# Optimization experiments

Hardware: AMD Instinct MI355X
Metric: run time of the kernel (lower is better)

## Reference

```python
import jax, jax.numpy as jnp
import numpy as np

B, D_MODEL, N, H = 4, 256, 2048, 4
HEAD_DIM = D_MODEL // H  # 64


def _rotate_half(x):
    # x: [..., d] with d even; pairs (x1, x2) -> (-x2, x1)
    x = x.reshape(x.shape[:-1] + (x.shape[-1] // 2, 2))
    x1, x2 = x[..., 0], x[..., 1]
    return jnp.stack((-x2, x1), axis=-1).reshape(x.shape[:-2] + (-1,))


def _apply_rope(freqs, t):
    # freqs: [2, n, d] (cos, sin); t: [b, h, n, d]
    return t * freqs[0] + _rotate_half(t) * freqs[1]


def setup_inputs() -> dict:
    key = jax.random.key(0)
    ks = jax.random.split(key, 12)
    s = 0.02
    inp = {
        "query": jax.random.normal(ks[0], (B, D_MODEL, N), jnp.float32),
        "key": jax.random.normal(ks[1], (B, D_MODEL, N), jnp.float32),
        "value": jax.random.normal(ks[2], (B, D_MODEL, N), jnp.float32),
        "encoding": jax.random.normal(ks[3], (2, N, HEAD_DIM), jnp.float32),
        "Wq": jax.random.normal(ks[4], (D_MODEL, D_MODEL), jnp.float32) * s,
        "bq": jnp.zeros((D_MODEL,), jnp.float32),
        "Wk": jax.random.normal(ks[5], (D_MODEL, D_MODEL), jnp.float32) * s,
        "bk": jnp.zeros((D_MODEL,), jnp.float32),
        "Wv": jax.random.normal(ks[6], (D_MODEL, D_MODEL), jnp.float32) * s,
        "bv": jnp.zeros((D_MODEL,), jnp.float32),
        "Wm": jax.random.normal(ks[7], (D_MODEL, D_MODEL), jnp.float32) * s,
        "bm": jnp.zeros((D_MODEL,), jnp.float32),
    }
    return inp


def _proj(W, b, x):
    # 1x1 Conv1d == channel matmul: x [b, c_in, n] -> [b, c_out, n]
    return jnp.einsum('oi,bin->bon', W, x) + b[None, :, None]


def reference(query, key, value, encoding, Wq, bq, Wk, bk, Wv, bv, Wm, bm):
    b = query.shape[0]
    # project and split channels into (head_dim, heads): [b, d, h, n]
    q = _proj(Wq, bq, query).reshape(b, HEAD_DIM, H, -1)
    k = _proj(Wk, bk, key).reshape(b, HEAD_DIM, H, -1)
    v = _proj(Wv, bv, value).reshape(b, HEAD_DIM, H, -1)
    # RoPE on [b, h, n, d] layout
    q = jnp.transpose(_apply_rope(encoding, jnp.transpose(q, (0, 2, 3, 1))), (0, 3, 1, 2))
    k = jnp.transpose(_apply_rope(encoding, jnp.transpose(k, (0, 2, 3, 1))), (0, 3, 1, 2))
    # attention: scores [b, h, n, m]
    scores = jnp.einsum('bdhn,bdhm->bhnm', q, k) / jnp.sqrt(jnp.float32(HEAD_DIM))
    prob = jax.nn.softmax(scores, axis=-1)
    x = jnp.einsum('bhnm,bdhm->bdhn', prob, v)
    x = x.reshape(b, HEAD_DIM * H, -1)
    return _proj(Wm, bm, x)
```

## Files before the change

kernel.cpp:

```cpp
#include <hip/hip_runtime.h>
#include <stdint.h>

#define NSEQ 2048

typedef __attribute__((ext_vector_type(4))) float f32x4;
typedef __attribute__((ext_vector_type(8))) short s16x8;
typedef _Float16 f16x8 __attribute__((ext_vector_type(8)));

#define OFF_XT  0u
#define OFF_PO  0u
#define OFF_M   16777216u
#define OFF_L   17301504u
#define OFF_QR  17825792u
#define OFF_KR  22020096u
#define OFF_VT  26214400u

__device__ __forceinline__ short f2h(float f) {
  _Float16 h = (_Float16)f;
  return __builtin_bit_cast(short, h);
}
__device__ __forceinline__ float h2f(short s) {
  return (float)__builtin_bit_cast(_Float16, s);
}
__device__ __forceinline__ int swz128(int row, int slot) {
  return row * 128 + ((slot ^ (row & 7)) << 4);
}
#define MFMA(a, b, c) __builtin_amdgcn_mfma_f32_16x16x32_f16(a, b, c, 0, 0, 0)

__global__ __launch_bounds__(256) void k_trans(const float* __restrict__ q,
    const float* __restrict__ k, const float* __restrict__ v, char* __restrict__ ws) {
  int tensor = blockIdx.z >> 2, b = blockIdx.z & 3;
  const float* src = tensor == 0 ? q : (tensor == 1 ? k : v);
  short* dst = (short*)(ws + OFF_XT) + (tensor * 4 + b) * 524288;
  int n0 = blockIdx.x * 64, i0 = blockIdx.y * 64;
  __shared__ float tile[64][65];
  int t = threadIdx.x;
  int nl = t & 63, ib = (t >> 6) * 16;
#pragma unroll
  for (int r = 0; r < 16; ++r)
    tile[ib + r][nl] = src[(b * 256 + i0 + ib + r) * 2048 + n0 + nl];
  __syncthreads();
  int nr = t >> 2, ic = (t & 3) * 16;
  short tmp[16];
#pragma unroll
  for (int j = 0; j < 16; ++j) tmp[j] = f2h(tile[ic + j][nr]);
  short* dp = &dst[(n0 + nr) * 256 + i0 + ic];
  *(s16x8*)dp = *(const s16x8*)&tmp[0];
  *(s16x8*)(dp + 8) = *(const s16x8*)&tmp[8];
}

__global__ __launch_bounds__(256) void k_proj(const float* __restrict__ Wq,
    const float* __restrict__ Wk, const float* __restrict__ Wv,
    const float* __restrict__ enc, const float* __restrict__ bq,
    const float* __restrict__ bk, const float* __restrict__ bv, char* __restrict__ ws) {
  int proj = blockIdx.z >> 2, b = blockIdx.z & 3;
  const float* W = proj == 0 ? Wq : (proj == 1 ? Wk : Wv);
  const short* X = (const short*)(ws + OFF_XT) + (proj * 4 + b) * 524288;
  int o0 = blockIdx.y * 64, n0 = blockIdx.x * 64;
  __shared__ short As[64 * 64], Bs[64 * 64];
  int t = threadIdx.x, lane = t & 63, g = lane >> 4, c = lane & 15, wave = t >> 6;
  int wr = wave >> 1, wc = wave & 1;
  int row = t >> 2, seg = t & 3;
  f32x4 acc[2][2] = {};
  for (int kk = 0; kk < 4; ++kk) {
    __syncthreads();
    int koff = kk * 64;
    const float* wsrc = &W[(o0 + row) * 256 + koff + seg * 16];
    short ha[16];
#pragma unroll
    for (int q4 = 0; q4 < 4; ++q4) {
      f32x4 wv4 = *(const f32x4*)(wsrc + q4 * 4);
#pragma unroll
      for (int j = 0; j < 4; ++j) ha[q4 * 4 + j] = f2h(wv4[j]);
    }
    *(s16x8*)((char*)As + swz128(row, seg * 2))     = *(const s16x8*)&ha[0];
    *(s16x8*)((char*)As + swz128(row, seg * 2 + 1)) = *(const s16x8*)&ha[8];
    const short* xsrc = &X[(n0 + row) * 256 + koff];
    *(s16x8*)((char*)Bs + swz128(row, seg))     = *(const s16x8*)(xsrc + seg * 8);
    *(s16x8*)((char*)Bs + swz128(row, 4 + seg)) = *(const s16x8*)(xsrc + 32 + seg * 8);
    __syncthreads();
#pragma unroll
    for (int ks = 0; ks < 2; ++ks) {
      f16x8 af[2], bfr[2];
#pragma unroll
      for (int f = 0; f < 2; ++f) {
        af[f]  = *(const f16x8*)((char*)As + swz128(wr * 32 + f * 16 + c, ks * 4 + g));
        bfr[f] = *(const f16x8*)((char*)Bs + swz128(wc * 32 + f * 16 + c, ks * 4 + g));
      }
#pragma unroll
      for (int i = 0; i < 2; ++i)
#pragma unroll
        for (int j = 0; j < 2; ++j)
          acc[i][j] = MFMA(af[i], bfr[j], acc[i][j]);
    }
  }
  const float* bias = proj == 0 ? bq : (proj == 1 ? bk : bv);
  if (proj < 2) {
    short* dst0 = (short*)(ws + (proj == 0 ? OFF_QR : OFF_KR));
    float scale = proj == 0 ? 0.18033688f : 1.0f;
    float sgn = (g & 1) ? 1.0f : -1.0f;
#pragma unroll
    for (int i = 0; i < 2; ++i) {
      int ob = o0 + wr * 32 + i * 16 + g * 4;
      int d = ob >> 2;
#pragma unroll
      for (int j = 0; j < 2; ++j) {
        int n = n0 + wc * 32 + j * 16 + c;
        float cv = enc[n * 64 + d], sv = enc[131072 + n * 64 + d];
#pragma unroll
        for (int r = 0; r < 4; ++r) {
          float val = acc[i][j][r] + bias[ob + r];
          float par = __shfl_xor(val, 16, 64);
          float res = (val * cv + sgn * par * sv) * scale;
          dst0[((b * 4 + r) * 2048 + n) * 64 + d] = f2h(res);
        }
      }
    }
  } else {
    short* dst = (short*)(ws + OFF_VT);
#pragma unroll
    for (int i = 0; i < 2; ++i) {
      int ob = o0 + wr * 32 + i * 16 + g * 4;
      int d = ob >> 2;
#pragma unroll
      for (int j = 0; j < 2; ++j) {
        int n = n0 + wc * 32 + j * 16 + c;
#pragma unroll
        for (int r = 0; r < 4; ++r) {
          float val = acc[i][j][r] + bias[ob + r];
          dst[((b * 4 + r) * 64 + d) * 2048 + n] = f2h(val);
        }
      }
    }
  }
}

__global__ __launch_bounds__(256, 4) void k_attn(char* __restrict__ ws) {
  int bh = blockIdx.y, ms = blockIdx.z;
  int t = threadIdx.x, wave = t >> 6, lane = t & 63, g = lane >> 4, c = lane & 15;
  int nw = blockIdx.x * 64 + wave * 16;
  const short* Q = (const short*)(ws + OFF_QR) + bh * 131072;
  const short* K = (const short*)(ws + OFF_KR) + bh * 131072;
  const short* V = (const short*)(ws + OFF_VT) + bh * 131072;
  __shared__ short Ks[64 * 64], Vs[64 * 64], Ps[4][16 * 64];
  char* Pb = (char*)Ps[wave];
  f16x8 qf0 = *(const f16x8*)&Q[(nw + c) * 64 + g * 8];
  f16x8 qf1 = *(const f16x8*)&Q[(nw + c) * 64 + 32 + g * 8];
  f32x4 po[4] = {};
  float mrun = -1e30f, lrun = 0.f;
  int sr = t >> 3, sl = t & 7;
  const int mb = ms * 512;
  int bsrc = g * 16 + g * 4;

  s16x8 RA[4], RB[4];
  auto LD = [&](int m0, s16x8* R) {
    R[0] = *(const s16x8*)&K[(m0 + sr) * 64 + sl * 8];
    R[1] = *(const s16x8*)&K[(m0 + sr + 32) * 64 + sl * 8];
    R[2] = *(const s16x8*)&V[sr * 2048 + m0 + sl * 8];
    R[3] = *(const s16x8*)&V[(sr + 32) * 2048 + m0 + sl * 8];
  };
  auto ST = [&](const s16x8* R) {
    *(s16x8*)((char*)Ks + swz128(sr, sl))      = R[0];
    *(s16x8*)((char*)Ks + swz128(sr + 32, sl)) = R[1];
    *(s16x8*)((char*)Vs + swz128(sr, sl))      = R[2];
    *(s16x8*)((char*)Vs + swz128(sr + 32, sl)) = R[3];
  };
  auto COMPUTE = [&]() {
    f32x4 s[4] = {};
    __builtin_amdgcn_s_setprio(1);
#pragma unroll
    for (int fj = 0; fj < 4; ++fj) {
      f16x8 k0 = *(const f16x8*)((char*)Ks + swz128(fj * 16 + c, g));
      f16x8 k1 = *(const f16x8*)((char*)Ks + swz128(fj * 16 + c, 4 + g));
      s[fj] = MFMA(k0, qf0, s[fj]);
      s[fj] = MFMA(k1, qf1, s[fj]);
    }
    __builtin_amdgcn_s_setprio(0);
    float t0 = fmaxf(fmaxf(s[0][0], s[0][1]), fmaxf(s[0][2], s[0][3]));
    float t1 = fmaxf(fmaxf(s[1][0], s[1][1]), fmaxf(s[1][2], s[1][3]));
    float t2 = fmaxf(fmaxf(s[2][0], s[2][1]), fmaxf(s[2][2], s[2][3]));
    float t3 = fmaxf(fmaxf(s[3][0], s[3][1]), fmaxf(s[3][2], s[3][3]));
    float rmax = fmaxf(fmaxf(t0, t1), fmaxf(t2, t3));
    rmax = fmaxf(rmax, __shfl_xor(rmax, 16, 64));
    rmax = fmaxf(rmax, __shfl_xor(rmax, 32, 64));
    if (__any(rmax > mrun + 11.5f)) {
      float nm = fmaxf(mrun, rmax);
      float corr = exp2f(mrun - nm);
      mrun = nm;
      lrun *= corr;
#pragma unroll
      for (int r = 0; r < 4; ++r) {
        float corr_r = __shfl(corr, bsrc + r, 64);
#pragma unroll
        for (int fd = 0; fd < 4; ++fd) po[fd][r] *= corr_r;
      }
    }
    float p[4][4], rs = 0.f;
#pragma unroll
    for (int fj = 0; fj < 4; ++fj) {
      f32x4 pv;
#pragma unroll
      for (int r = 0; r < 4; ++r) {
        pv[r] = exp2f(s[fj][r] - mrun);
        p[fj][r] = pv[r];
      }
      rs += (pv[0] + pv[1]) + (pv[2] + pv[3]);
    }
    rs += __shfl_xor(rs, 16, 64);
    rs += __shfl_xor(rs, 32, 64);
    lrun += rs;
#pragma unroll
    for (int fj = 0; fj < 4; ++fj)
#pragma unroll
      for (int r = 0; r < 4; ++r) {
        int mm = fj * 16 + g * 4 + r;
        *(short*)(Pb + swz128(c, mm >> 3) + (mm & 7) * 2) = f2h(p[fj][r]);
      }
    asm volatile("s_waitcnt lgkmcnt(0)" ::: "memory");
    __builtin_amdgcn_sched_barrier(0);
    f16x8 pa0 = *(const f16x8*)(Pb + swz128(c, g));
    f16x8 pa1 = *(const f16x8*)(Pb + swz128(c, 4 + g));
    __builtin_amdgcn_s_setprio(1);
#pragma unroll
    for (int fd = 0; fd < 4; ++fd) {
      int dd = fd * 16 + c;
      f16x8 vb0 = *(const f16x8*)((char*)Vs + swz128(dd, g));
      f16x8 vb1 = *(const f16x8*)((char*)Vs + swz128(dd, 4 + g));
      po[fd] = MFMA(pa0, vb0, po[fd]);
      po[fd] = MFMA(pa1, vb1, po[fd]);
    }
    __builtin_amdgcn_s_setprio(0);
  };

  LD(mb, RA);
  for (int tt = 0; tt < 8; tt += 2) {
    __syncthreads();
    ST(RA);
    LD(mb + (tt + 1) * 64, RB);
    __syncthreads();
    COMPUTE();
    __syncthreads();
    ST(RB);
    if (tt + 2 < 8) LD(mb + (tt + 2) * 64, RA);
    __syncthreads();
    COMPUTE();
  }

  short* PO = (short*)(ws + OFF_PO);
  float* Mm = (float*)(ws + OFF_M);
  float* Ll = (float*)(ws + OFF_L);
  int base = (ms * 16 + bh) * 2048;
  float li[4];
#pragma unroll
  for (int r = 0; r < 4; ++r) li[r] = 1.0f / __shfl(lrun, bsrc + r, 64);
#pragma unroll
  for (int fd = 0; fd < 4; ++fd) {
    int d = fd * 16 + c;
#pragma unroll
    for (int r = 0; r < 4; ++r) {
      int n = nw + g * 4 + r;
      PO[(base + n) * 64 + d] = f2h(po[fd][r] * li[r]);
    }
  }
  if (g == 0) {
    Mm[base + nw + c] = mrun;
    Ll[base + nw + c] = lrun;
  }
}

__global__ __launch_bounds__(256) void k_final(const float* __restrict__ Wm,
    const float* __restrict__ bm, float* __restrict__ out, char* __restrict__ ws) {
  int b = blockIdx.z;
  int o0 = blockIdx.y * 64, n0 = blockIdx.x * 64;
  const short* PO = (const short*)(ws + OFF_PO);
  const float* Mm = (const float*)(ws + OFF_M);
  const float* Ll = (const float*)(ws + OFF_L);
  __shared__ short As[64 * 64], Bs[64 * 64];
  int t = threadIdx.x, lane = t & 63, g = lane >> 4, c = lane & 15, wave = t >> 6;
  int wr = wave >> 1, wc = wave & 1;
  int row = t >> 2, seg = t & 3;
  f32x4 acc[2][2] = {};
  for (int kk = 0; kk < 4; ++kk) {
    __syncthreads();
    short ha[16];
#pragma unroll
    for (int j = 0; j < 16; ++j)
      ha[j] = f2h(Wm[(o0 + row) * 256 + (seg * 16 + j) * 4 + kk]);
    *(s16x8*)((char*)As + swz128(row, seg * 2))     = *(const s16x8*)&ha[0];
    *(s16x8*)((char*)As + swz128(row, seg * 2 + 1)) = *(const s16x8*)&ha[8];
    int bh = b * 4 + kk;
    int nr = n0 + row;
    float m0 = Mm[(0 * 16 + bh) * 2048 + nr], l0 = Ll[(0 * 16 + bh) * 2048 + nr];
    float m1 = Mm[(1 * 16 + bh) * 2048 + nr], l1 = Ll[(1 * 16 + bh) * 2048 + nr];
    float m2 = Mm[(2 * 16 + bh) * 2048 + nr], l2 = Ll[(2 * 16 + bh) * 2048 + nr];
    float m3 = Mm[(3 * 16 + bh) * 2048 + nr], l3 = Ll[(3 * 16 + bh) * 2048 + nr];
    float M = fmaxf(fmaxf(m0, m1), fmaxf(m2, m3));
    float w0 = l0 * exp2f(m0 - M), w1 = l1 * exp2f(m1 - M);
    float w2 = l2 * exp2f(m2 - M), w3 = l3 * exp2f(m3 - M);
    float inv = 1.f / (w0 + w1 + w2 + w3);
    w0 *= inv; w1 *= inv; w2 *= inv; w3 *= inv;
    float cb[16];
    {
      const short* p0 = &PO[((0 * 16 + bh) * 2048 + nr) * 64 + seg * 16];
      const short* p1 = &PO[((1 * 16 + bh) * 2048 + nr) * 64 + seg * 16];
      const short* p2 = &PO[((2 * 16 + bh) * 2048 + nr) * 64 + seg * 16];
      const short* p3 = &PO[((3 * 16 + bh) * 2048 + nr) * 64 + seg * 16];
      s16x8 a0 = *(const s16x8*)p0, a1 = *(const s16x8*)(p0 + 8);
      s16x8 b0 = *(const s16x8*)p1, b1 = *(const s16x8*)(p1 + 8);
      s16x8 c0 = *(const s16x8*)p2, c1 = *(const s16x8*)(p2 + 8);
      s16x8 d0 = *(const s16x8*)p3, d1 = *(const s16x8*)(p3 + 8);
#pragma unroll
      for (int j = 0; j < 8; ++j) {
        cb[j]     = w0 * h2f(a0[j]) + w1 * h2f(b0[j]) + w2 * h2f(c0[j]) + w3 * h2f(d0[j]);
        cb[j + 8] = w0 * h2f(a1[j]) + w1 * h2f(b1[j]) + w2 * h2f(c1[j]) + w3 * h2f(d1[j]);
      }
    }
    short hb[16];
#pragma unroll
    for (int j = 0; j < 16; ++j) hb[j] = f2h(cb[j]);
    *(s16x8*)((char*)Bs + swz128(row, seg * 2))     = *(const s16x8*)&hb[0];
    *(s16x8*)((char*)Bs + swz128(row, seg * 2 + 1)) = *(const s16x8*)&hb[8];
    __syncthreads();
#pragma unroll
    for (int ks = 0; ks < 2; ++ks) {
      f16x8 af[2], bfr[2];
#pragma unroll
      for (int f = 0; f < 2; ++f) {
        af[f]  = *(const f16x8*)((char*)As + swz128(wr * 32 + f * 16 + c, ks * 4 + g));
        bfr[f] = *(const f16x8*)((char*)Bs + swz128(wc * 32 + f * 16 + c, ks * 4 + g));
      }
#pragma unroll
      for (int i = 0; i < 2; ++i)
#pragma unroll
        for (int j = 0; j < 2; ++j)
          acc[i][j] = MFMA(af[i], bfr[j], acc[i][j]);
    }
  }
#pragma unroll
  for (int i = 0; i < 2; ++i) {
    int ob = o0 + wr * 32 + i * 16 + g * 4;
#pragma unroll
    for (int j = 0; j < 2; ++j) {
      int n = n0 + wc * 32 + j * 16 + c;
#pragma unroll
      for (int r = 0; r < 4; ++r)
        out[(b * 256 + ob + r) * 2048 + n] = acc[i][j][r] + bm[ob + r];
    }
  }
}

extern "C" void kernel_launch(void* const* d_in, const int* in_sizes, int n_in,
                              void* d_out, int out_size, void* d_ws, size_t ws_size,
                              hipStream_t stream) {
  (void)in_sizes; (void)n_in; (void)out_size; (void)ws_size;
  const float* q   = (const float*)d_in[0];
  const float* k   = (const float*)d_in[1];
  const float* v   = (const float*)d_in[2];
  const float* enc = (const float*)d_in[3];
  const float* Wq  = (const float*)d_in[4];
  const float* bq  = (const float*)d_in[5];
  const float* Wk  = (const float*)d_in[6];
  const float* bk  = (const float*)d_in[7];
  const float* Wv  = (const float*)d_in[8];
  const float* bv  = (const float*)d_in[9];
  const float* Wm  = (const float*)d_in[10];
  const float* bm  = (const float*)d_in[11];
  char* ws = (char*)d_ws;
  float* out = (float*)d_out;
  hipLaunchKernelGGL(k_trans, dim3(32, 4, 12), dim3(256), 0, stream, q, k, v, ws);
  hipLaunchKernelGGL(k_proj, dim3(32, 4, 12), dim3(256), 0, stream, Wq, Wk, Wv, enc, bq, bk, bv, ws);
  hipLaunchKernelGGL(k_attn, dim3(32, 16, 4), dim3(256), 0, stream, ws);
  hipLaunchKernelGGL(k_final, dim3(32, 4, 4), dim3(256), 0, stream, Wm, bm, out, ws);
}
```

Measured before the change: 161.1 us.

## Pre-convert weights to fp16, stage attention output via LDS, retile final projection

Adds a kernel that converts all four weight matrices to fp16 once per call, with Wm pre-permuted, so the projection and final kernels load fp16 weights with vector loads instead of converting per block or doing strided gathers. The attention epilogue now writes the normalized partial output into shared memory (Pb) and then stores it to global memory with 16-byte coalesced writes, replacing scattered 2-byte stores. k_final is retiled to 64x32 output tiles, doubling the grid, and both GEMM kernels remap block IDs for an XCD-aware ordering. The cost is one extra kernel launch and the risk that the Pb buffer reuse in k_attn conflicts with data still live in shared memory.

```diff
diff --git a/kernel.cpp b/kernel.cpp
--- a/kernel.cpp
+++ b/kernel.cpp
@@ -14,6 +14,7 @@
 #define OFF_QR  17825792u
 #define OFF_KR  22020096u
 #define OFF_VT  26214400u
+#define OFF_W   30408704u
 
 __device__ __forceinline__ short f2h(float f) {
   _Float16 h = (_Float16)f;
@@ -26,6 +27,16 @@
   return row * 128 + ((slot ^ (row & 7)) << 4);
 }
 #define MFMA(a, b, c) __builtin_amdgcn_mfma_f32_16x16x32_f16(a, b, c, 0, 0, 0)
+
+__global__ void k_convw(const float* __restrict__ Wq, const float* __restrict__ Wk,
+                        const float* __restrict__ Wv, const float* __restrict__ Wm,
+                        char* __restrict__ ws) {
+  int o = blockIdx.x, which = blockIdx.y, i = threadIdx.x;
+  const float* src = which == 0 ? Wq : which == 1 ? Wk : which == 2 ? Wv : Wm;
+  short* dst = (short*)(ws + OFF_W) + which * 65536;
+  float val = (which < 3) ? src[o * 256 + i] : src[o * 256 + ((i & 63) << 2) + (i >> 6)];
+  dst[o * 256 + i] = f2h(val);
+}
 
 __global__ __launch_bounds__(256) void k_trans(const float* __restrict__ q,
     const float* __restrict__ k, const float* __restrict__ v, char* __restrict__ ws) {
@@ -49,14 +60,16 @@
   *(s16x8*)(dp + 8) = *(const s16x8*)&tmp[8];
 }
 
-__global__ __launch_bounds__(256) void k_proj(const float* __restrict__ Wq,
-    const float* __restrict__ Wk, const float* __restrict__ Wv,
-    const float* __restrict__ enc, const float* __restrict__ bq,
-    const float* __restrict__ bk, const float* __restrict__ bv, char* __restrict__ ws) {
-  int proj = blockIdx.z >> 2, b = blockIdx.z & 3;
-  const float* W = proj == 0 ? Wq : (proj == 1 ? Wk : Wv);
+__global__ __launch_bounds__(256) void k_proj(const float* __restrict__ enc,
+    const float* __restrict__ bq, const float* __restrict__ bk,
+    const float* __restrict__ bv, char* __restrict__ ws) {
+  int hid = blockIdx.x + 32 * (blockIdx.y + 4 * blockIdx.z);
+  int fm = (hid & 7) * 192 + (hid >> 3);
+  int yo = fm & 3, xn = (fm >> 2) & 31, z = fm >> 7;
+  int proj = z >> 2, b = z & 3;
+  const short* W = (const short*)(ws + OFF_W) + proj * 65536;
   const short* X = (const short*)(ws + OFF_XT) + (proj * 4 + b) * 524288;
-  int o0 = blockIdx.y * 64, n0 = blockIdx.x * 64;
+  int o0 = yo * 64, n0 = xn * 64;
   __shared__ short As[64 * 64], Bs[64 * 64];
   int t = threadIdx.x, lane = t & 63, g = lane >> 4, c = lane & 15, wave = t >> 6;
   int wr = wave >> 1, wc = wave & 1;
@@ -65,17 +78,10 @@
   for (int kk = 0; kk < 4; ++kk) {
     __syncthreads();
     int koff = kk * 64;
-    const float* wsrc = &W[(o0 + row) * 256 + koff + seg * 16];
-    short ha[16];
-#pragma unroll
-    for (int q4 = 0; q4 < 4; ++q4) {
-      f32x4 wv4 = *(const f32x4*)(wsrc + q4 * 4);
-#pragma unroll
-      for (int j = 0; j < 4; ++j) ha[q4 * 4 + j] = f2h(wv4[j]);
-    }
-    *(s16x8*)((char*)As + swz128(row, seg * 2))     = *(const s16x8*)&ha[0];
-    *(s16x8*)((char*)As + swz128(row, seg * 2 + 1)) = *(const s16x8*)&ha[8];
+    const short* wsrc = &W[(o0 + row) * 256 + koff];
     const short* xsrc = &X[(n0 + row) * 256 + koff];
+    *(s16x8*)((char*)As + swz128(row, seg))     = *(const s16x8*)(wsrc + seg * 8);
+    *(s16x8*)((char*)As + swz128(row, 4 + seg)) = *(const s16x8*)(wsrc + 32 + seg * 8);
     *(s16x8*)((char*)Bs + swz128(row, seg))     = *(const s16x8*)(xsrc + seg * 8);
     *(s16x8*)((char*)Bs + swz128(row, 4 + seg)) = *(const s16x8*)(xsrc + 32 + seg * 8);
     __syncthreads();
@@ -253,43 +259,51 @@
   float li[4];
 #pragma unroll
   for (int r = 0; r < 4; ++r) li[r] = 1.0f / __shfl(lrun, bsrc + r, 64);
+  asm volatile("s_waitcnt lgkmcnt(0)" ::: "memory");
+  __builtin_amdgcn_sched_barrier(0);
 #pragma unroll
   for (int fd = 0; fd < 4; ++fd) {
     int d = fd * 16 + c;
 #pragma unroll
-    for (int r = 0; r < 4; ++r) {
-      int n = nw + g * 4 + r;
-      PO[(base + n) * 64 + d] = f2h(po[fd][r] * li[r]);
-    }
-  }
+    for (int r = 0; r < 4; ++r)
+      *(short*)(Pb + swz128(g * 4 + r, d >> 3) + (d & 7) * 2) = f2h(po[fd][r] * li[r]);
+  }
+  asm volatile("s_waitcnt lgkmcnt(0)" ::: "memory");
+  __builtin_amdgcn_sched_barrier(0);
+  int rr = lane >> 2, ds = (lane & 3) * 16;
+  s16x8 v0 = *(const s16x8*)(Pb + swz128(rr, ds >> 3));
+  s16x8 v1 = *(const s16x8*)(Pb + swz128(rr, (ds >> 3) + 1));
+  *(s16x8*)&PO[(base + nw + rr) * 64 + ds]     = v0;
+  *(s16x8*)&PO[(base + nw + rr) * 64 + ds + 8] = v1;
   if (g == 0) {
     Mm[base + nw + c] = mrun;
     Ll[base + nw + c] = lrun;
   }
 }
 
-__global__ __launch_bounds__(256) void k_final(const float* __restrict__ Wm,
-    const float* __restrict__ bm, float* __restrict__ out, char* __restrict__ ws) {
-  int b = blockIdx.z;
-  int o0 = blockIdx.y * 64, n0 = blockIdx.x * 64;
+__global__ __launch_bounds__(256) void k_final(const float* __restrict__ bm,
+    float* __restrict__ out, char* __restrict__ ws) {
+  int hid = blockIdx.x + 64 * (blockIdx.y + 4 * blockIdx.z);
+  int fm = (hid & 7) * 128 + (hid >> 3);
+  int yo = fm & 3, xn = (fm >> 2) & 63, b = fm >> 8;
+  int o0 = yo * 64, n0 = xn * 32;
+  const short* Wf = (const short*)(ws + OFF_W) + 3 * 65536;
   const short* PO = (const short*)(ws + OFF_PO);
   const float* Mm = (const float*)(ws + OFF_M);
   const float* Ll = (const float*)(ws + OFF_L);
-  __shared__ short As[64 * 64], Bs[64 * 64];
+  __shared__ short As[64 * 64], Bs[32 * 64];
   int t = threadIdx.x, lane = t & 63, g = lane >> 4, c = lane & 15, wave = t >> 6;
   int wr = wave >> 1, wc = wave & 1;
-  int row = t >> 2, seg = t & 3;
-  f32x4 acc[2][2] = {};
+  int arow = t >> 2, aseg = t & 3;
+  int brow = t >> 3, bseg = t & 7;
+  f32x4 acc[2] = {};
   for (int kk = 0; kk < 4; ++kk) {
     __syncthreads();
-    short ha[16];
-#pragma unroll
-    for (int j = 0; j < 16; ++j)
-      ha[j] = f2h(Wm[(o0 + row) * 256 + (seg * 16 + j) * 4 + kk]);
-    *(s16x8*)((char*)As + swz128(row, seg * 2))     = *(const s16x8*)&ha[0];
-    *(s16x8*)((char*)As + swz128(row, seg * 2 + 1)) = *(const s16x8*)&ha[8];
+    const short* wsrc = &Wf[(o0 + arow) * 256 + kk * 64];
+    *(s16x8*)((char*)As + swz128(arow, aseg))     = *(const s16x8*)(wsrc + aseg * 8);
+    *(s16x8*)((char*)As + swz128(arow, 4 + aseg)) = *(const s16x8*)(wsrc + 32 + aseg * 8);
     int bh = b * 4 + kk;
-    int nr = n0 + row;
+    int nr = n0 + brow;
     float m0 = Mm[(0 * 16 + bh) * 2048 + nr], l0 = Ll[(0 * 16 + bh) * 2048 + nr];
     float m1 = Mm[(1 * 16 + bh) * 2048 + nr], l1 = Ll[(1 * 16 + bh) * 2048 + nr];
     float m2 = Mm[(2 * 16 + bh) * 2048 + nr], l2 = Ll[(2 * 16 + bh) * 2048 + nr];
@@ -299,53 +313,35 @@
     float w2 = l2 * exp2f(m2 - M), w3 = l3 * exp2f(m3 - M);
     float inv = 1.f / (w0 + w1 + w2 + w3);
     w0 *= inv; w1 *= inv; w2 *= inv; w3 *= inv;
-    float cb[16];
-    {
-      const short* p0 = &PO[((0 * 16 + bh) * 2048 + nr) * 64 + seg * 16];
-      const short* p1 = &PO[((1 * 16 + bh) * 2048 + nr) * 64 + seg * 16];
-      const short* p2 = &PO[((2 * 16 + bh) * 2048 + nr) * 64 + seg * 16];
-      const short* p3 = &PO[((3 * 16 + bh) * 2048 + nr) * 64 + seg * 16];
-      s16x8 a0 = *(const s16x8*)p0, a1 = *(const s16x8*)(p0 + 8);
-      s16x8 b0 = *(const s16x8*)p1, b1 = *(const s16x8*)(p1 + 8);
-      s16x8 c0 = *(const s16x8*)p2, c1 = *(const s16x8*)(p2 + 8);
-      s16x8 d0 = *(const s16x8*)p3, d1 = *(const s16x8*)(p3 + 8);
-#pragma unroll
-      for (int j = 0; j < 8; ++j) {
-        cb[j]     = w0 * h2f(a0[j]) + w1 * h2f(b0[j]) + w2 * h2f(c0[j]) + w3 * h2f(d0[j]);
-        cb[j + 8] = w0 * h2f(a1[j]) + w1 * h2f(b1[j]) + w2 * h2f(c1[j]) + w3 * h2f(d1[j]);
-      }
-    }
-    short hb[16];
-#pragma unroll
-    for (int j = 0; j < 16; ++j) hb[j] = f2h(cb[j]);
-    *(s16x8*)((char*)Bs + swz128(row, seg * 2))     = *(const s16x8*)&hb[0];
-    *(s16x8*)((char*)Bs + swz128(row, seg * 2 + 1)) = *(const s16x8*)&hb[8];
+    s16x8 a0 = *(const s16x8*)&PO[((0 * 16 + bh) * 2048 + nr) * 64 + bseg * 8];
+    s16x8 a1 = *(const s16x8*)&PO[((1 * 16 + bh) * 2048 + nr) * 64 + bseg * 8];
+    s16x8 a2 = *(const s16x8*)&PO[((2 * 16 + bh) * 2048 + nr) * 64 + bseg * 8];
+    s16x8 a3 = *(const s16x8*)&PO[((3 * 16 + bh) * 2048 + nr) * 64 + bseg * 8];
+    short hb[8];
+#pragma unroll
+    for (int j = 0; j < 8; ++j)
+      hb[j] = f2h(w0 * h2f(a0[j]) + w1 * h2f(a1[j]) + w2 * h2f(a2[j]) + w3 * h2f(a3[j]));
+    *(s16x8*)((char*)Bs + swz128(brow, bseg)) = *(const s16x8*)hb;
     __syncthreads();
 #pragma unroll
     for (int ks = 0; ks < 2; ++ks) {
-      f16x8 af[2], bfr[2];
-#pragma unroll
-      for (int f = 0; f < 2; ++f) {
-        af[f]  = *(const f16x8*)((char*)As + swz128(wr * 32 + f * 16 + c, ks * 4 + g));
-        bfr[f] = *(const f16x8*)((char*)Bs + swz128(wc * 32 + f * 16 + c, ks * 4 + g));
-      }
+      f16x8 af[2], bfr;
+#pragma unroll
+      for (int f = 0; f < 2; ++f)
+        af[f] = *(const f16x8*)((char*)As + swz128(wr * 32 + f * 16 + c, ks * 4 + g));
+      bfr = *(const f16x8*)((char*)Bs + swz128(wc * 16 + c, ks * 4 + g));
 #pragma unroll
       for (int i = 0; i < 2; ++i)
-#pragma unroll
-        for (int j = 0; j < 2; ++j)
-          acc[i][j] = MFMA(af[i], bfr[j], acc[i][j]);
+        acc[i] = MFMA(af[i], bfr, acc[i]);
     }
   }
 #pragma unroll
   for (int i = 0; i < 2; ++i) {
     int ob = o0 + wr * 32 + i * 16 + g * 4;
-#pragma unroll
-    for (int j = 0; j < 2; ++j) {
-      int n = n0 + wc * 32 + j * 16 + c;
-#pragma unroll
-      for (int r = 0; r < 4; ++r)
-        out[(b * 256 + ob + r) * 2048 + n] = acc[i][j][r] + bm[ob + r];
-    }
+    int n = n0 + wc * 16 + c;
+#pragma unroll
+    for (int r = 0; r < 4; ++r)
+      out[(b * 256 + ob + r) * 2048 + n] = acc[i][r] + bm[ob + r];
   }
 }
 
@@ -367,8 +363,9 @@
   const float* bm  = (const float*)d_in[11];
   char* ws = (char*)d_ws;
   float* out = (float*)d_out;
+  hipLaunchKernelGGL(k_convw, dim3(256, 4), dim3(256), 0, stream, Wq, Wk, Wv, Wm, ws);
   hipLaunchKernelGGL(k_trans, dim3(32, 4, 12), dim3(256), 0, stream, q, k, v, ws);
-  hipLaunchKernelGGL(k_proj, dim3(32, 4, 12), dim3(256), 0, stream, Wq, Wk, Wv, enc, bq, bk, bv, ws);
+  hipLaunchKernelGGL(k_proj, dim3(32, 4, 12), dim3(256), 0, stream, enc, bq, bk, bv, ws);
   hipLaunchKernelGGL(k_attn, dim3(32, 16, 4), dim3(256), 0, stream, ws);
-  hipLaunchKernelGGL(k_final, dim3(32, 4, 4), dim3(256), 0, stream, Wm, bm, out, ws);
-}
+  hipLaunchKernelGGL(k_final, dim3(64, 4, 4), dim3(256), 0, stream, bm, out, ws);
+}
```

After: 161.9 us. About the same (+0.5%).
